# Kernel tuning notes

Hardware: AMD Instinct MI355X
Metric: run time of the kernel (lower is better)

## Reference

```python
import jax, jax.numpy as jnp
import numpy as np
from jax import lax

B, N, F = 64, 768, 256
P, T, K = 64, 16, 3  # per_lead, after_lead, kernel_size


def setup_inputs() -> dict:
    key = jax.random.key(0)
    k1, k2, k3, k4, k5 = jax.random.split(key, 5)
    x = jax.random.normal(k1, (B, N, F), dtype=jnp.float32)
    adj = jax.random.uniform(k2, (B, N, N), dtype=jnp.float32)
    fan_in = P * 1 * K
    bound = 1.0 / np.sqrt(fan_in)
    conv_w = jax.random.uniform(k3, (T, P, 1, K), minval=-bound, maxval=bound, dtype=jnp.float32)
    conv_b = jax.random.uniform(k4, (T,), minval=-bound, maxval=bound, dtype=jnp.float32)
    re_param = jax.random.normal(k5, (K, 1), dtype=jnp.float32)
    return {"x": x, "adj": adj, "conv_w": conv_w, "conv_b": conv_b, "re_param": re_param}


def reference(x, adj, conv_w, conv_b, re_param):
    b, n, f = x.shape
    t, p, _, k = conv_w.shape
    L = n // p  # number of leads
    # feature pooling: [B, P, L, F] -conv(1,k)-> [B, T, L, F]
    x4 = x.reshape(b, p, L, f)
    pad = (k - 1) // 2
    y = lax.conv_general_dilated(
        x4, conv_w, window_strides=(1, 1), padding=[(0, 0), (pad, pad)],
        dimension_numbers=("NCHW", "OIHW", "NCHW"))
    y = y + conv_b[None, :, None, None]
    pooled_x = y.reshape(b, t * L, f)
    # assignment matrix s = conv_w @ re_param  -> [T, P]
    s = jnp.einsum("tpik,kj->tp", conv_w, re_param)
    # block-diagonal coarsening: for every (lead_i, lead_j) block do s @ A_ij @ s^T
    adj5 = adj.reshape(b, L, p, L, p)
    pooled = jnp.einsum("tp,blpmq,uq->bltmu", s, adj5, s)
    pooled_adj = pooled.reshape(b, L * t, L * t)
    return pooled_x, pooled_adj
```

## Files before the change

kernel.cpp:

```cpp
#include <hip/hip_runtime.h>

#define B_ 64
#define N_ 768
#define F_ 256
#define P_ 64
#define T_ 16
#define K_ 3
#define L_ 12

__global__ __launch_bounds__(256) void pool_x_kernel(
    const float* __restrict__ x, const float* __restrict__ conv_w,
    const float* __restrict__ conv_b, float* __restrict__ out)
{
    __shared__ float xt[P_][F_];
    const int blk = blockIdx.x;
    const int b = blk / L_, l = blk % L_;
    const int f = threadIdx.x;

    const float* xb = x + (size_t)b * N_ * F_ + (size_t)l * F_;
    #pragma unroll 8
    for (int p = 0; p < P_; ++p) {
        xt[p][f] = xb[(size_t)p * (L_ * F_) + f];
    }
    __syncthreads();

    float acc[T_];
    #pragma unroll
    for (int t = 0; t < T_; ++t) acc[t] = conv_b[t];

    for (int p = 0; p < P_; ++p) {
        const float xm = (f > 0)      ? xt[p][f - 1] : 0.f;
        const float x0 = xt[p][f];
        const float xp = (f < F_ - 1) ? xt[p][f + 1] : 0.f;
        const float* wp = conv_w + p * K_;
        #pragma unroll
        for (int t = 0; t < T_; ++t) {
            const float w0 = wp[t * (P_ * K_) + 0];
            const float w1 = wp[t * (P_ * K_) + 1];
            const float w2 = wp[t * (P_ * K_) + 2];
            acc[t] = fmaf(xm, w0, fmaf(x0, w1, fmaf(xp, w2, acc[t])));
        }
    }

    float* ob = out + (size_t)b * (T_ * L_) * F_ + f;
    #pragma unroll
    for (int t = 0; t < T_; ++t) {
        ob[(size_t)(t * L_ + l) * F_] = acc[t];
    }
}

#define SSTRIDE 68
#define TSTRIDE 772

__global__ __launch_bounds__(256) void pool_adj_kernel(
    const float* __restrict__ adj, const float* __restrict__ conv_w,
    const float* __restrict__ re_param, float* __restrict__ out)
{
    __shared__ float s_lds[T_][SSTRIDE];
    __shared__ float tmp[T_][TSTRIDE];

    const int blk = blockIdx.x;
    const int b = blk / L_, l = blk % L_;
    const int tid = threadIdx.x;

    const float r0 = re_param[0], r1 = re_param[1], r2 = re_param[2];
    for (int i = tid; i < T_ * P_; i += 256) {
        const int t = i / P_, p = i % P_;
        const float* w = conv_w + (size_t)i * K_;
        s_lds[t][p] = w[0] * r0 + w[1] * r1 + w[2] * r2;
    }
    __syncthreads();

    float acc0[T_], acc1[T_], acc2[T_];
    #pragma unroll
    for (int t = 0; t < T_; ++t) { acc0[t] = 0.f; acc1[t] = 0.f; acc2[t] = 0.f; }

    const float* ab = adj + (size_t)b * N_ * N_ + (size_t)(l * P_) * N_;
    for (int p = 0; p < P_; ++p) {
        const float* row = ab + (size_t)p * N_;
        const float a0 = row[tid];
        const float a1 = row[tid + 256];
        const float a2 = row[tid + 512];
        #pragma unroll
        for (int t = 0; t < T_; ++t) {
            const float sv = s_lds[t][p];
            acc0[t] = fmaf(sv, a0, acc0[t]);
            acc1[t] = fmaf(sv, a1, acc1[t]);
            acc2[t] = fmaf(sv, a2, acc2[t]);
        }
    }
    #pragma unroll
    for (int t = 0; t < T_; ++t) {
        tmp[t][tid]       = acc0[t];
        tmp[t][tid + 256] = acc1[t];
        tmp[t][tid + 512] = acc2[t];
    }
    __syncthreads();

    const int t = tid >> 4, u = tid & 15;
    float sum[L_];
    #pragma unroll
    for (int m = 0; m < L_; ++m) sum[m] = 0.f;
    for (int q = 0; q < P_; ++q) {
        const float sq = s_lds[u][q];
        #pragma unroll
        for (int m = 0; m < L_; ++m)
            sum[m] = fmaf(tmp[t][m * P_ + q], sq, sum[m]);
    }

    float* ob = out + (size_t)b * (L_ * T_) * (L_ * T_)
                    + (size_t)(l * T_ + t) * (L_ * T_) + u;
    #pragma unroll
    for (int m = 0; m < L_; ++m)
        ob[m * T_] = sum[m];
}

extern "C" void kernel_launch(void* const* d_in, const int* in_sizes, int n_in,
                              void* d_out, int out_size, void* d_ws, size_t ws_size,
                              hipStream_t stream) {
    (void)in_sizes; (void)n_in; (void)out_size; (void)d_ws; (void)ws_size;
    const float* x        = (const float*)d_in[0];
    const float* adj      = (const float*)d_in[1];
    const float* conv_w   = (const float*)d_in[2];
    const float* conv_b   = (const float*)d_in[3];
    const float* re_param = (const float*)d_in[4];

    float* pooled_x   = (float*)d_out;
    float* pooled_adj = (float*)d_out + (size_t)B_ * (T_ * L_) * F_;

    pool_x_kernel<<<B_ * L_, 256, 0, stream>>>(x, conv_w, conv_b, pooled_x);
    pool_adj_kernel<<<B_ * L_, 256, 0, stream>>>(adj, conv_w, re_param, pooled_adj);
}
```

Baseline: 86.00 us.

## Fuse x-pooling and adj-pooling into one launch with float4 adj tiling

Merges the two kernels into a single launch that gives alternating blocks the x-conv role or the adj-coarsening role, so the two memory-bound phases overlap on the GPU instead of running back to back. The x path drops its shared-memory staging and reads neighbours straight from global memory. The adj path now loads float4 vectors, and each wave covers 4 t values times 12 columns. The second contraction reads tmp as float4 and uses a transposed s table. The cost is that every block now reserves the large tmp shared array, x blocks included, which may lower occupancy, and the x path makes redundant overlapping global loads.

```diff
diff --git a/kernel.cpp b/kernel.cpp
--- a/kernel.cpp
+++ b/kernel.cpp
@@ -7,93 +7,101 @@
 #define T_ 16
 #define K_ 3
 #define L_ 12
+#define TSTRIDE 772
 
-__global__ __launch_bounds__(256) void pool_x_kernel(
-    const float* __restrict__ x, const float* __restrict__ conv_w,
-    const float* __restrict__ conv_b, float* __restrict__ out)
+__global__ __launch_bounds__(256) void fused_pool_kernel(
+    const float* __restrict__ x, const float* __restrict__ adj,
+    const float* __restrict__ conv_w, const float* __restrict__ conv_b,
+    const float* __restrict__ re_param,
+    float* __restrict__ out_x, float* __restrict__ out_adj)
 {
-    __shared__ float xt[P_][F_];
-    const int blk = blockIdx.x;
-    const int b = blk / L_, l = blk % L_;
-    const int f = threadIdx.x;
+    __shared__ float sT[P_][T_];
+    __shared__ float tmp[T_][TSTRIDE];
 
-    const float* xb = x + (size_t)b * N_ * F_ + (size_t)l * F_;
-    #pragma unroll 8
-    for (int p = 0; p < P_; ++p) {
-        xt[p][f] = xb[(size_t)p * (L_ * F_) + f];
+    const int blk  = blockIdx.x;
+    const int role = blk & 1;
+    const int idx  = blk >> 1;
+    const int b = idx / L_, l = idx % L_;
+    const int tid = threadIdx.x;
+
+    if (role == 1) {
+        const int f = tid;
+        const float* xb = x + (size_t)b * N_ * F_ + (size_t)l * F_;
+
+        float acc[T_];
+        #pragma unroll
+        for (int t = 0; t < T_; ++t) acc[t] = conv_b[t];
+
+        for (int p = 0; p < P_; ++p) {
+            const float* row = xb + (size_t)p * (L_ * F_);
+            const float xm = (f > 0)      ? row[f - 1] : 0.f;
+            const float x0 = row[f];
+            const float xp = (f < F_ - 1) ? row[f + 1] : 0.f;
+            const float* wp = conv_w + p * K_;
+            #pragma unroll
+            for (int t = 0; t < T_; ++t) {
+                const float w0 = wp[t * (P_ * K_) + 0];
+                const float w1 = wp[t * (P_ * K_) + 1];
+                const float w2 = wp[t * (P_ * K_) + 2];
+                acc[t] = fmaf(xm, w0, fmaf(x0, w1, fmaf(xp, w2, acc[t])));
+            }
+        }
+        float* ob = out_x + (size_t)b * (T_ * L_) * F_ + f;
+        #pragma unroll
+        for (int t = 0; t < T_; ++t)
+            ob[(size_t)(t * L_ + l) * F_] = acc[t];
+        return;
+    }
+
+    const float r0 = re_param[0], r1 = re_param[1], r2 = re_param[2];
+    for (int i = tid; i < P_ * T_; i += 256) {
+        const int p = i >> 4, t = i & 15;
+        const float* wv = conv_w + (size_t)t * (P_ * K_) + (size_t)p * K_;
+        sT[p][t] = wv[0] * r0 + wv[1] * r1 + wv[2] * r2;
     }
     __syncthreads();
 
-    float acc[T_];
+    const int w  = tid >> 6;
+    const int ct = tid & 63;
+
+    float acc[4][12];
     #pragma unroll
-    for (int t = 0; t < T_; ++t) acc[t] = conv_b[t];
-
-    for (int p = 0; p < P_; ++p) {
-        const float xm = (f > 0)      ? xt[p][f - 1] : 0.f;
-        const float x0 = xt[p][f];
-        const float xp = (f < F_ - 1) ? xt[p][f + 1] : 0.f;
-        const float* wp = conv_w + p * K_;
+    for (int j = 0; j < 4; ++j)
         #pragma unroll
-        for (int t = 0; t < T_; ++t) {
-            const float w0 = wp[t * (P_ * K_) + 0];
-            const float w1 = wp[t * (P_ * K_) + 1];
-            const float w2 = wp[t * (P_ * K_) + 2];
-            acc[t] = fmaf(xm, w0, fmaf(x0, w1, fmaf(xp, w2, acc[t])));
-        }
-    }
-
-    float* ob = out + (size_t)b * (T_ * L_) * F_ + f;
-    #pragma unroll
-    for (int t = 0; t < T_; ++t) {
-        ob[(size_t)(t * L_ + l) * F_] = acc[t];
-    }
-}
-
-#define SSTRIDE 68
-#define TSTRIDE 772
-
-__global__ __launch_bounds__(256) void pool_adj_kernel(
-    const float* __restrict__ adj, const float* __restrict__ conv_w,
-    const float* __restrict__ re_param, float* __restrict__ out)
-{
-    __shared__ float s_lds[T_][SSTRIDE];
-    __shared__ float tmp[T_][TSTRIDE];
-
-    const int blk = blockIdx.x;
-    const int b = blk / L_, l = blk % L_;
-    const int tid = threadIdx.x;
-
-    const float r0 = re_param[0], r1 = re_param[1], r2 = re_param[2];
-    for (int i = tid; i < T_ * P_; i += 256) {
-        const int t = i / P_, p = i % P_;
-        const float* w = conv_w + (size_t)i * K_;
-        s_lds[t][p] = w[0] * r0 + w[1] * r1 + w[2] * r2;
-    }
-    __syncthreads();
-
-    float acc0[T_], acc1[T_], acc2[T_];
-    #pragma unroll
-    for (int t = 0; t < T_; ++t) { acc0[t] = 0.f; acc1[t] = 0.f; acc2[t] = 0.f; }
+        for (int c = 0; c < 12; ++c) acc[j][c] = 0.f;
 
     const float* ab = adj + (size_t)b * N_ * N_ + (size_t)(l * P_) * N_;
     for (int p = 0; p < P_; ++p) {
         const float* row = ab + (size_t)p * N_;
-        const float a0 = row[tid];
-        const float a1 = row[tid + 256];
-        const float a2 = row[tid + 512];
+        const float4 a0 = *(const float4*)&row[ct * 4];
+        const float4 a1 = *(const float4*)&row[ct * 4 + 256];
+        const float4 a2 = *(const float4*)&row[ct * 4 + 512];
         #pragma unroll
-        for (int t = 0; t < T_; ++t) {
-            const float sv = s_lds[t][p];
-            acc0[t] = fmaf(sv, a0, acc0[t]);
-            acc1[t] = fmaf(sv, a1, acc1[t]);
-            acc2[t] = fmaf(sv, a2, acc2[t]);
+        for (int j = 0; j < 4; ++j) {
+            const float sv = sT[p][4 * w + j];
+            acc[j][0]  = fmaf(sv, a0.x, acc[j][0]);
+            acc[j][1]  = fmaf(sv, a0.y, acc[j][1]);
+            acc[j][2]  = fmaf(sv, a0.z, acc[j][2]);
+            acc[j][3]  = fmaf(sv, a0.w, acc[j][3]);
+            acc[j][4]  = fmaf(sv, a1.x, acc[j][4]);
+            acc[j][5]  = fmaf(sv, a1.y, acc[j][5]);
+            acc[j][6]  = fmaf(sv, a1.z, acc[j][6]);
+            acc[j][7]  = fmaf(sv, a1.w, acc[j][7]);
+            acc[j][8]  = fmaf(sv, a2.x, acc[j][8]);
+            acc[j][9]  = fmaf(sv, a2.y, acc[j][9]);
+            acc[j][10] = fmaf(sv, a2.z, acc[j][10]);
+            acc[j][11] = fmaf(sv, a2.w, acc[j][11]);
         }
     }
     #pragma unroll
-    for (int t = 0; t < T_; ++t) {
-        tmp[t][tid]       = acc0[t];
-        tmp[t][tid + 256] = acc1[t];
-        tmp[t][tid + 512] = acc2[t];
+    for (int j = 0; j < 4; ++j) {
+        #pragma unroll
+        for (int i = 0; i < 3; ++i) {
+            float4 v;
+            v.x = acc[j][i * 4 + 0]; v.y = acc[j][i * 4 + 1];
+            v.z = acc[j][i * 4 + 2]; v.w = acc[j][i * 4 + 3];
+            *(float4*)&tmp[4 * w + j][ct * 4 + i * 256] = v;
+        }
     }
     __syncthreads();
 
@@ -101,15 +109,21 @@
     float sum[L_];
     #pragma unroll
     for (int m = 0; m < L_; ++m) sum[m] = 0.f;
-    for (int q = 0; q < P_; ++q) {
-        const float sq = s_lds[u][q];
+
+    for (int q4 = 0; q4 < P_; q4 += 4) {
+        const float s0 = sT[q4 + 0][u];
+        const float s1 = sT[q4 + 1][u];
+        const float s2 = sT[q4 + 2][u];
+        const float s3 = sT[q4 + 3][u];
         #pragma unroll
-        for (int m = 0; m < L_; ++m)
-            sum[m] = fmaf(tmp[t][m * P_ + q], sq, sum[m]);
+        for (int m = 0; m < L_; ++m) {
+            const float4 tv = *(const float4*)&tmp[t][m * P_ + q4];
+            sum[m] = fmaf(tv.x, s0, fmaf(tv.y, s1, fmaf(tv.z, s2, fmaf(tv.w, s3, sum[m]))));
+        }
     }
 
-    float* ob = out + (size_t)b * (L_ * T_) * (L_ * T_)
-                    + (size_t)(l * T_ + t) * (L_ * T_) + u;
+    float* ob = out_adj + (size_t)b * (L_ * T_) * (L_ * T_)
+                        + (size_t)(l * T_ + t) * (L_ * T_) + u;
     #pragma unroll
     for (int m = 0; m < L_; ++m)
         ob[m * T_] = sum[m];
@@ -128,6 +142,6 @@
     float* pooled_x   = (float*)d_out;
     float* pooled_adj = (float*)d_out + (size_t)B_ * (T_ * L_) * F_;
 
-    pool_x_kernel<<<B_ * L_, 256, 0, stream>>>(x, conv_w, conv_b, pooled_x);
-    pool_adj_kernel<<<B_ * L_, 256, 0, stream>>>(adj, conv_w, re_param, pooled_adj);
+    fused_pool_kernel<<<B_ * L_ * 2, 256, 0, stream>>>(
+        x, adj, conv_w, conv_b, re_param, pooled_x, pooled_adj);
 }
```

Result: faster. 76.12 us (-11.5%).
